# Kernel tuning notes

Measured on AMD Instinct MI355X. Metric: run time of the kernel, lower is better.

Reference implementation:

```python
import jax, jax.numpy as jnp
import numpy as np
import math

B, N, T, CI, CO = 4, 2048, 64, 32, 32
K, TAU = 6, 3


def _cheb(x, gso, k_order):
    # x: [b,n,t,c] complex, gso: [n,n] complex -> [K,b,n,t,c]
    polys = [x]
    if k_order > 1:
        polys.append(jnp.einsum('nm,bmtc->bntc', gso, x))
    for _ in range(2, k_order):
        polys.append(2.0 * jnp.einsum('nm,bmtc->bntc', gso, polys[-1]) - polys[-2])
    return jnp.stack(polys)


def _lag(p, tau):
    # shift along time axis (-2) by tau, zero-padding at the front
    if tau == 0:
        return p
    pad = jnp.zeros_like(p[..., :tau, :])
    return jnp.concatenate([pad, p[..., :-tau, :]], axis=-2)


def setup_inputs() -> dict:
    key = jax.random.key(0)
    ks = jax.random.split(key, 6)
    scale = 1.0 / math.sqrt(K * TAU * CI)
    gso_scale = 0.5 / math.sqrt(N)  # keep spectral radius ~<=1 for Cheb recursion
    return {
        'x_real': jax.random.normal(ks[0], (B, N, T, CI), jnp.float32),
        'x_imag': jax.random.normal(ks[1], (B, N, T, CI), jnp.float32),
        'gso_real': jax.random.normal(ks[2], (N, N), jnp.float32) * gso_scale,
        'gso_imag': jax.random.normal(ks[3], (N, N), jnp.float32) * gso_scale,
        'weight_real': jax.random.uniform(ks[4], (K, TAU, CI, CO), jnp.float32, -scale, scale),
        'weight_imag': jax.random.uniform(ks[5], (K, TAU, CI, CO), jnp.float32, -scale, scale),
        'bias_real': jnp.zeros((CO,), jnp.float32),
        'bias_imag': jnp.zeros((CO,), jnp.float32),
    }


def reference(x_real, x_imag, gso_real, gso_imag, weight_real, weight_imag, bias_real, bias_imag):
    x = jax.lax.complex(x_real, x_imag)
    gso = jax.lax.complex(gso_real, gso_imag)
    w = jax.lax.complex(weight_real, weight_imag)  # [K,TAU,i,o]
    bias = jax.lax.complex(bias_real, bias_imag)
    # Lag (time shift) and the graph shift act on different axes, so they
    # commute: compute the Chebyshev recursion ONCE on x, then lag the
    # stacked polynomials — same math as cheb(lag(x)) in the original.
    polys = _cheb(x, gso, K)  # [K,b,n,t,c]
    out = jnp.zeros((B, N, T, CO), dtype=polys.dtype)
    for tau in range(TAU):
        out = out + jnp.einsum('kbnti,kio->bnto', _lag(polys, tau), w[:, tau])
    return out + bias
```

## Files before the change

kernel.cpp:

```cpp
#include <hip/hip_runtime.h>
#include <stdint.h>

#define Bn 4
#define Nn 2048
#define Tn 64
#define CIn 32
#define COn 32
#define Kn 6
#define TAUn 3
#define Jn 8192

typedef _Float16 f16;
typedef _Float16 f16x2 __attribute__((ext_vector_type(2)));
typedef _Float16 f16x4 __attribute__((ext_vector_type(4)));
typedef _Float16 f16x8 __attribute__((ext_vector_type(8)));
typedef float f32x4 __attribute__((ext_vector_type(4)));

template <int N> struct ic { static constexpr int v = N; };

#if defined(__has_builtin)
#if __has_builtin(__builtin_amdgcn_fdot2)
#define HAVE_FDOT2 1
#endif
#endif

__device__ __forceinline__ float fdot2(f16x2 a, f16x2 b, float c) {
#ifdef HAVE_FDOT2
  return __builtin_amdgcn_fdot2(a, b, c, false);
#else
  return c + (float)a[0] * (float)b[0] + (float)a[1] * (float)b[1];
#endif
}

__device__ __forceinline__ void gld_lds16(const void* g, void* l) {
  auto gp = (const __attribute__((address_space(1))) uint32_t*)(uintptr_t)g;
  auto lp = (__attribute__((address_space(3))) uint32_t*)(uint32_t)(uintptr_t)l;
  __builtin_amdgcn_global_load_lds(gp, lp, 16, 0, 0);
}

__global__ __launch_bounds__(256) void pack_gso(const float* __restrict__ gr,
                                                const float* __restrict__ gi,
                                                f16* __restrict__ Gr,
                                                f16* __restrict__ Gi) {
  int u = blockIdx.x * 256 + threadIdx.x;
  float4 vr = ((const float4*)gr)[u];
  float4 vi = ((const float4*)gi)[u];
  f16x4 hr, hi;
  hr[0] = (f16)vr.x; hr[1] = (f16)vr.y; hr[2] = (f16)vr.z; hr[3] = (f16)vr.w;
  hi[0] = (f16)vi.x; hi[1] = (f16)vi.y; hi[2] = (f16)vi.z; hi[3] = (f16)vi.w;
  ((f16x4*)Gr)[u] = hr;
  ((f16x4*)Gi)[u] = hi;
}

__global__ __launch_bounds__(256) void pack_x(const float* __restrict__ xr,
                                              const float* __restrict__ xi,
                                              f16* __restrict__ P0) {
  __shared__ float tile[64][65];
  const int t = threadIdx.x;
  const int q0 = blockIdx.x * 64;
  const int n0 = blockIdx.y * 64;
  const int b = blockIdx.z;
  const int rr = t >> 4;
  const int cc = (t & 15) * 4;
  #pragma unroll
  for (int plane = 0; plane < 2; ++plane) {
    const float* src = plane ? xi : xr;
    if (plane) __syncthreads();
    #pragma unroll
    for (int it = 0; it < 4; ++it) {
      int n = it * 16 + rr;
      float4 v = *(const float4*)(src + ((size_t)b * Nn + n0 + n) * 2048 + q0 + cc);
      tile[n][cc + 0] = v.x; tile[n][cc + 1] = v.y;
      tile[n][cc + 2] = v.z; tile[n][cc + 3] = v.w;
    }
    __syncthreads();
    #pragma unroll
    for (int it = 0; it < 4; ++it) {
      int q = it * 16 + rr;
      f16x4 hv;
      hv[0] = (f16)tile[cc + 0][q];
      hv[1] = (f16)tile[cc + 1][q];
      hv[2] = (f16)tile[cc + 2][q];
      hv[3] = (f16)tile[cc + 3][q];
      *(f16x4*)(P0 + ((size_t)b * 2048 + q0 + q) * 4096 + plane * 2048 + n0 + cc) = hv;
    }
  }
}

__global__ __launch_bounds__(256) void pack_w(const float* __restrict__ wr,
                                              const float* __restrict__ wi,
                                              uint2* __restrict__ wpk) {
  int idx = blockIdx.x * 256 + threadIdx.x;
  if (idx >= Kn * TAUn * CIn * COn) return;
  float r = wr[idx], i = wi[idx];
  uint16_t hr = __builtin_bit_cast(uint16_t, (f16)r);
  uint16_t hi = __builtin_bit_cast(uint16_t, (f16)i);
  uint16_t hni = __builtin_bit_cast(uint16_t, (f16)(-i));
  uint2 o;
  o.x = (uint32_t)hr | ((uint32_t)hni << 16);
  o.y = (uint32_t)hi | ((uint32_t)hr << 16);
  wpk[idx] = o;
}

template <int MODE>
__global__ __launch_bounds__(256, 2) void cheb_gemm(
    const f16* __restrict__ Gr, const f16* __restrict__ Gi,
    const f16* __restrict__ P, f16* __restrict__ Q) {
  extern __shared__ __align__(16) char lds[];
  f16* L = (f16*)lds;

  const int tid = threadIdx.x;
  const int lane = tid & 63;
  const int w = tid >> 6;
  const int wm = w >> 1;
  const int wn = w & 1;
  const int sub = lane >> 4, rr = lane & 15;

  const int bid = blockIdx.x;
  const int xcd = bid & 7;
  const int l = bid >> 3;
  const int s = l & 63, wv = l >> 6;
  const int bj = xcd * 8 + (s >> 3);
  const int bn = (s & 7) + 8 * wv;
  const int n0 = bn * 128, j0 = bj * 128;
  const bool top = n0 < 2048;
  const int gmbase = n0 & 2047;

  const int trow = tid >> 3;
  const int cg = (tid & 7) ^ (trow & 7);
  const size_t aoffg = (size_t)(gmbase + trow) * 2048 + cg * 8;
  const size_t boffg = (size_t)(j0 + trow) * 4096 + cg * 8;
  const int sdst = w * 512;

  const int arb = rr * 64 + (sub ^ (rr & 3)) * 8;
  const int x32 = ((rr >> 2) & 1) * 32;
  const int kofs[2] = {x32, 32 - x32};

  auto stageA = [&](const f16* plane, int kcol, int h, int slot) {
    #pragma unroll
    for (int p = 0; p < 2; ++p)
      gld_lds16(plane + aoffg + h * 131072 + p * 65536 + kcol,
                L + slot * 4096 + sdst + p * 2048);
  };
  auto stageB = [&](int kt_, int h, int slot) {
    #pragma unroll
    for (int p = 0; p < 2; ++p)
      gld_lds16(P + boffg + h * 262144 + p * 131072 + kt_ * 64,
                L + slot * 4096 + sdst + p * 2048);
  };
  auto Aplane = [&](int kt_) -> const f16* {
    bool kr = (kt_ & 32) != 0;
    return top ? (kr ? Gi : Gr) : (kr ? Gr : Gi);
  };

  f32x4 acc[4][4] = {};
  f16x8 afr[2][2], bfr0[2][2], bfr1[2][2];

  stageB(0, 0, 2);
  stageA(Aplane(0), 0, 0, 0);
  stageA(Aplane(0), 0, 1, 1);
  stageB(0, 1, 3);
  stageB(1, 0, 6);
  stageA(Aplane(1), 64, 0, 4);

  for (int k2 = 0; k2 < 32; ++k2) {
    const int ktb = k2 * 2;

    auto tile = [&](auto ec) {
      constexpr int E = decltype(ec)::v;
      const int kt = ktb + E;
      const int ktn = (kt + 1) & 63;
      const int ktn2 = (kt + 2) & 63;
      const f16* apn = Aplane(ktn);
      const f16* apn2 = Aplane(ktn2);
      const int kcoln = (ktn * 64) & 2047;
      const int kcoln2 = (ktn2 * 64) & 2047;
      const bool negA = top && (kt & 32);

      auto loadA = [&](int qm) {
        #pragma unroll
        for (int f = 0; f < 2; ++f)
          #pragma unroll
          for (int ks = 0; ks < 2; ++ks)
            afr[f][ks] = *(const f16x8*)(
                L + (E * 4 + wm) * 4096 + qm * 2048 + f * 1024 + arb + kofs[ks]);
        if (negA) {
          #pragma unroll
          for (int f = 0; f < 2; ++f) { afr[f][0] = -afr[f][0]; afr[f][1] = -afr[f][1]; }
        }
      };
      auto loadB = [&](f16x8 (&bq)[2][2], int qn) {
        #pragma unroll
        for (int fc = 0; fc < 2; ++fc)
          #pragma unroll
          for (int ks = 0; ks < 2; ++ks)
            bq[fc][ks] = *(const f16x8*)(
                L + (E * 4 + 2 + wn) * 4096 + qn * 2048 + fc * 1024 + arb + kofs[ks]);
      };
      auto mf16 = [&](f16x8 (&bq)[2][2], int accR, int accC) {
        __builtin_amdgcn_s_setprio(1);
        #pragma unroll
        for (int ks = 0; ks < 2; ++ks)
          #pragma unroll
          for (int f = 0; f < 2; ++f)
            #pragma unroll
            for (int fc = 0; fc < 2; ++fc)
              acc[accR + f][accC + fc] = __builtin_amdgcn_mfma_f32_16x16x32_f16(
                  afr[f][ks], bq[fc][ks], acc[accR + f][accC + fc], 0, 0, 0);
        __builtin_amdgcn_s_setprio(0);
      };

      asm volatile("s_waitcnt vmcnt(4)" ::: "memory");
      __builtin_amdgcn_s_barrier();

      loadA(0); loadB(bfr0, 0);
      stageA(apn, kcoln, 1, (E ^ 1) * 4 + 1);
      mf16(bfr0, 0, 0);

      loadB(bfr1, 1);
      stageB(ktn, 1, (E ^ 1) * 4 + 3);
      mf16(bfr1, 0, 2);

      loadA(1);
      asm volatile("s_waitcnt lgkmcnt(0)" ::: "memory");
      __builtin_amdgcn_s_barrier();
      stageB(ktn2, 0, E * 4 + 2);
      mf16(bfr1, 2, 2);

      stageA(apn2, kcoln2, 0, E * 4 + 0);
      mf16(bfr0, 2, 0);
    };

    tile(ic<0>{});
    tile(ic<1>{});
  }

  asm volatile("s_waitcnt vmcnt(0)" ::: "memory");

  #pragma unroll
  for (int fc = 0; fc < 4; ++fc) {
    size_t j = (size_t)j0 + wn * 64 + fc * 16 + (lane & 15);
    #pragma unroll
    for (int fr = 0; fr < 4; ++fr) {
      int nn = n0 + wm * 64 + fr * 16 + ((lane >> 4) << 2);
      size_t off = j * 4096 + nn;
      f16x4 v;
      if (MODE == 1) {
        f16x4 o = *(const f16x4*)(Q + off);
        #pragma unroll
        for (int r = 0; r < 4; ++r)
          v[r] = (f16)(2.0f * acc[fr][fc][r] - (float)o[r]);
      } else {
        #pragma unroll
        for (int r = 0; r < 4; ++r)
          v[r] = (f16)acc[fr][fc][r];
      }
      *(f16x4*)(Q + off) = v;
    }
  }
}

template <bool CPLX>
__global__ __launch_bounds__(256, 2) void contract_k(
    const f16* __restrict__ Pc, const uint2* __restrict__ wpk,
    const float* __restrict__ biasr, const float* __restrict__ biasi,
    float* __restrict__ out, int k) {
  __shared__ __align__(16) uint32_t Plds[192 * 64];
  __shared__ __align__(16) uint32_t WA[96 * 32];
  __shared__ __align__(16) uint32_t WB[CPLX ? 96 * 32 : 32];

  const int t = threadIdx.x;
  const int n0 = blockIdx.x * 64;
  const int t0 = blockIdx.y * 4;
  const int b = blockIdx.z;

  #pragma unroll
  for (int it = 0; it < 6; ++it) {
    int task = it * 256 + t;
    int row = task >> 3, oc = task & 7;
    int tp = (t0 - 2) * 32 + row;
    uint4 ur = {0, 0, 0, 0}, ui = {0, 0, 0, 0};
    if (tp >= 0) {
      size_t goff = ((size_t)b * 2048 + tp) * 4096 + n0 + oc * 8;
      ur = *(const uint4*)(Pc + goff);
      ui = *(const uint4*)(Pc + goff + 2048);
    }
    uint32_t* dst = &Plds[row * 64 + oc * 8];
    dst[0] = (ur.x & 0xffffu) | (ui.x << 16);
    dst[1] = (ur.x >> 16) | (ui.x & 0xffff0000u);
    dst[2] = (ur.y & 0xffffu) | (ui.y << 16);
    dst[3] = (ur.y >> 16) | (ui.y & 0xffff0000u);
    dst[4] = (ur.z & 0xffffu) | (ui.z << 16);
    dst[5] = (ur.z >> 16) | (ui.z & 0xffff0000u);
    dst[6] = (ur.w & 0xffffu) | (ui.w << 16);
    dst[7] = (ur.w >> 16) | (ui.w & 0xffff0000u);
  }
  #pragma unroll
  for (int it = 0; it < 12; ++it) {
    int idx = it * 256 + t;
    int q = idx >> 5, o = idx & 31;
    int tau = 2 - (q >> 5), ci = q & 31;
    uint2 wv = wpk[((k * TAUn + tau) * CIn + ci) * COn + o];
    WA[idx] = wv.x;
    if (CPLX) WB[idx] = wv.y;
  }
  __syncthreads();

  const int no = t & 7, ng = t >> 3;
  float aR[4][8] = {};
  float aI[4][8] = {};
  for (int q = 0; q < 96; ++q) {
    uint4 wa = *(const uint4*)&WA[q * 32 + no * 4];
    const uint32_t* wap = &wa.x;
    uint4 wb;
    const uint32_t* wbp = &wb.x;
    if (CPLX) wb = *(const uint4*)&WB[q * 32 + no * 4];
    #pragma unroll
    for (int ts = 0; ts < 4; ++ts) {
      uint2 pp = *(const uint2*)&Plds[(ts * 32 + q) * 64 + ng * 2];
      f16x2 h0 = __builtin_bit_cast(f16x2, pp.x);
      f16x2 h1 = __builtin_bit_cast(f16x2, pp.y);
      #pragma unroll
      for (int c = 0; c < 4; ++c) {
        f16x2 wv = __builtin_bit_cast(f16x2, wap[c]);
        aR[ts][c] = fdot2(h0, wv, aR[ts][c]);
        aR[ts][4 + c] = fdot2(h1, wv, aR[ts][4 + c]);
      }
      if (CPLX) {
        #pragma unroll
        for (int c = 0; c < 4; ++c) {
          f16x2 wv = __builtin_bit_cast(f16x2, wbp[c]);
          aI[ts][c] = fdot2(h0, wv, aI[ts][c]);
          aI[ts][4 + c] = fdot2(h1, wv, aI[ts][4 + c]);
        }
      }
    }
  }

  #pragma unroll
  for (int ts = 0; ts < 4; ++ts) {
    const int tt = t0 + ts;
    #pragma unroll
    for (int a = 0; a < 2; ++a) {
      size_t n = (size_t)n0 + ng * 2 + a;
      size_t ob = (((size_t)b * Nn + n) * Tn + tt) * COn + no * 4;
      if (!CPLX) {
        float4 v;
        v.x = aR[ts][a * 4 + 0]; v.y = aR[ts][a * 4 + 1];
        v.z = aR[ts][a * 4 + 2]; v.w = aR[ts][a * 4 + 3];
        float4 cur;
        if (k == 0) cur = *(const float4*)(biasr + no * 4);
        else cur = *(const float4*)(out + ob);
        v.x += cur.x; v.y += cur.y; v.z += cur.z; v.w += cur.w;
        *(float4*)(out + ob) = v;
      } else {
        float* po = out + ob * 2;
        float4 lo, hi;
        lo.x = aR[ts][a * 4 + 0]; lo.y = aI[ts][a * 4 + 0];
        lo.z = aR[ts][a * 4 + 1]; lo.w = aI[ts][a * 4 + 1];
        hi.x = aR[ts][a * 4 + 2]; hi.y = aI[ts][a * 4 + 2];
        hi.z = aR[ts][a * 4 + 3]; hi.w = aI[ts][a * 4 + 3];
        float4 c0, c1;
        if (k == 0) {
          const float* pr = biasr + no * 4;
          const float* pi = biasi + no * 4;
          c0 = make_float4(pr[0], pi[0], pr[1], pi[1]);
          c1 = make_float4(pr[2], pi[2], pr[3], pi[3]);
        } else {
          c0 = *(const float4*)(po);
          c1 = *(const float4*)(po + 4);
        }
        lo.x += c0.x; lo.y += c0.y; lo.z += c0.z; lo.w += c0.w;
        hi.x += c1.x; hi.y += c1.y; hi.z += c1.z; hi.w += c1.w;
        *(float4*)(po) = lo;
        *(float4*)(po + 4) = hi;
      }
    }
  }
}

extern "C" void kernel_launch(void* const* d_in, const int* in_sizes, int n_in,
                              void* d_out, int out_size, void* d_ws, size_t ws_size,
                              hipStream_t stream) {
  (void)in_sizes; (void)n_in;
  const float* xr = (const float*)d_in[0];
  const float* xi = (const float*)d_in[1];
  const float* gr = (const float*)d_in[2];
  const float* gi = (const float*)d_in[3];
  const float* wr = (const float*)d_in[4];
  const float* wi = (const float*)d_in[5];
  const float* biasr = (const float*)d_in[6];
  const float* biasi = (const float*)d_in[7];
  float* out = (float*)d_out;

  const size_t PPLANE = (size_t)Jn * 4096 * sizeof(f16);
  const size_t GPLANE = (size_t)Nn * Nn * sizeof(f16);
  const size_t WPK = (size_t)Kn * TAUn * CIn * COn * 8;
  if (ws_size < 2 * PPLANE + 2 * GPLANE + WPK) return;

  char* ws = (char*)d_ws;
  f16* P0 = (f16*)(ws);
  f16* P1 = (f16*)(ws + PPLANE);
  f16* Gr = (f16*)(ws + 2 * PPLANE);
  f16* Gi = (f16*)(ws + 2 * PPLANE + GPLANE);
  uint2* wpk = (uint2*)(ws + 2 * PPLANE + 2 * GPLANE);

  const bool cplx = (out_size == 2 * Bn * Nn * Tn * COn);

  pack_gso<<<dim3(4096), dim3(256), 0, stream>>>(gr, gi, Gr, Gi);
  pack_x<<<dim3(32, 32, 4), dim3(256), 0, stream>>>(xr, xi, P0);
  pack_w<<<dim3(72), dim3(256), 0, stream>>>(wr, wi, wpk);

  #define CONTRACT(KK, Pp)                                                         \
    do {                                                                           \
      if (cplx)                                                                    \
        contract_k<true><<<dim3(32, 16, 4), dim3(256), 0, stream>>>(               \
            Pp, wpk, biasr, biasi, out, KK);                                       \
      else                                                                         \
        contract_k<false><<<dim3(32, 16, 4), dim3(256), 0, stream>>>(              \
            Pp, wpk, biasr, biasi, out, KK);                                       \
    } while (0)

  CONTRACT(0, P0);
  cheb_gemm<0><<<dim3(2048), dim3(256), 65536, stream>>>(Gr, Gi, P0, P1);
  CONTRACT(1, P1);
  cheb_gemm<1><<<dim3(2048), dim3(256), 65536, stream>>>(Gr, Gi, P1, P0);
  CONTRACT(2, P0);
  cheb_gemm<1><<<dim3(2048), dim3(256), 65536, stream>>>(Gr, Gi, P0, P1);
  CONTRACT(3, P1);
  cheb_gemm<1><<<dim3(2048), dim3(256), 65536, stream>>>(Gr, Gi, P1, P0);
  CONTRACT(4, P0);
  cheb_gemm<1><<<dim3(2048), dim3(256), 65536, stream>>>(Gr, Gi, P0, P1);
  CONTRACT(5, P1);
  #undef CONTRACT
}
```

Baseline: 1.891 ms.

## Halve cheb_gemm K-tile and LDS footprint to raise occupancy to four blocks

The Chebyshev GEMM now stages 32-wide K tiles in a two-slot double buffer instead of 64-wide tiles in a more elaborately interleaved four-way staging scheme, halving dynamic LDS to 32KB. Launch bounds move from two to four blocks per CU so that more waves can hide memory latency. Each tile loads all A/B fragments, then issues a 4x4 block of MFMAs in one burst. The trade-off is twice as many loop iterations and barriers per output tile, and the loss of fine-grained overlap between LDS reads, global staging and MFMA issue. The tighter register cap may also cause spills.

Result: slower. 2.175 ms (+15.0%).

```diff
diff --git a/kernel.cpp b/kernel.cpp
--- a/kernel.cpp
+++ b/kernel.cpp
@@ -103,7 +103,7 @@
 }
 
 template <int MODE>
-__global__ __launch_bounds__(256, 2) void cheb_gemm(
+__global__ __launch_bounds__(256, 4) void cheb_gemm(
     const f16* __restrict__ Gr, const f16* __restrict__ Gi,
     const f16* __restrict__ P, f16* __restrict__ Q) {
   extern __shared__ __align__(16) char lds[];
@@ -126,109 +126,77 @@
   const bool top = n0 < 2048;
   const int gmbase = n0 & 2047;
 
-  const int trow = tid >> 3;
-  const int cg = (tid & 7) ^ (trow & 7);
-  const size_t aoffg = (size_t)(gmbase + trow) * 2048 + cg * 8;
-  const size_t boffg = (size_t)(j0 + trow) * 4096 + cg * 8;
+  const int srow = tid >> 2;
+  const int kcg = (tid & 3) ^ ((tid >> 3) & 3);
+  const size_t aoffg = (size_t)(gmbase + srow) * 2048 + kcg * 8;
+  const size_t boffg = (size_t)(j0 + srow) * 4096 + kcg * 8;
   const int sdst = w * 512;
 
-  const int arb = rr * 64 + (sub ^ (rr & 3)) * 8;
-  const int x32 = ((rr >> 2) & 1) * 32;
-  const int kofs[2] = {x32, 32 - x32};
-
-  auto stageA = [&](const f16* plane, int kcol, int h, int slot) {
+  const int arb = rr * 32 + (sub ^ ((rr >> 1) & 3)) * 8;
+
+  auto stageA = [&](const f16* plane, int kcol, int slot) {
     #pragma unroll
     for (int p = 0; p < 2; ++p)
-      gld_lds16(plane + aoffg + h * 131072 + p * 65536 + kcol,
-                L + slot * 4096 + sdst + p * 2048);
+      gld_lds16(plane + aoffg + p * 131072 + kcol,
+                L + slot * 4096 + p * 2048 + sdst);
   };
-  auto stageB = [&](int kt_, int h, int slot) {
+  auto stageB = [&](int kt_, int slot) {
     #pragma unroll
     for (int p = 0; p < 2; ++p)
-      gld_lds16(P + boffg + h * 262144 + p * 131072 + kt_ * 64,
-                L + slot * 4096 + sdst + p * 2048);
+      gld_lds16(P + boffg + p * 262144 + kt_ * 32,
+                L + slot * 4096 + p * 2048 + sdst);
   };
   auto Aplane = [&](int kt_) -> const f16* {
-    bool kr = (kt_ & 32) != 0;
+    bool kr = (kt_ & 64) != 0;
     return top ? (kr ? Gi : Gr) : (kr ? Gr : Gi);
   };
 
   f32x4 acc[4][4] = {};
-  f16x8 afr[2][2], bfr0[2][2], bfr1[2][2];
-
-  stageB(0, 0, 2);
-  stageA(Aplane(0), 0, 0, 0);
-  stageA(Aplane(0), 0, 1, 1);
-  stageB(0, 1, 3);
-  stageB(1, 0, 6);
-  stageA(Aplane(1), 64, 0, 4);
-
-  for (int k2 = 0; k2 < 32; ++k2) {
+  f16x8 afr[4], bfr[4];
+
+  stageA(Aplane(0), 0, 0);
+  stageB(0, 2);
+  stageA(Aplane(1), 32, 1);
+  stageB(1, 3);
+
+  for (int k2 = 0; k2 < 64; ++k2) {
     const int ktb = k2 * 2;
 
     auto tile = [&](auto ec) {
       constexpr int E = decltype(ec)::v;
       const int kt = ktb + E;
-      const int ktn = (kt + 1) & 63;
-      const int ktn2 = (kt + 2) & 63;
-      const f16* apn = Aplane(ktn);
+      const int ktn2 = (kt + 2) & 127;
       const f16* apn2 = Aplane(ktn2);
-      const int kcoln = (ktn * 64) & 2047;
-      const int kcoln2 = (ktn2 * 64) & 2047;
-      const bool negA = top && (kt & 32);
-
-      auto loadA = [&](int qm) {
-        #pragma unroll
-        for (int f = 0; f < 2; ++f)
-          #pragma unroll
-          for (int ks = 0; ks < 2; ++ks)
-            afr[f][ks] = *(const f16x8*)(
-                L + (E * 4 + wm) * 4096 + qm * 2048 + f * 1024 + arb + kofs[ks]);
-        if (negA) {
-          #pragma unroll
-          for (int f = 0; f < 2; ++f) { afr[f][0] = -afr[f][0]; afr[f][1] = -afr[f][1]; }
-        }
-      };
-      auto loadB = [&](f16x8 (&bq)[2][2], int qn) {
-        #pragma unroll
-        for (int fc = 0; fc < 2; ++fc)
-          #pragma unroll
-          for (int ks = 0; ks < 2; ++ks)
-            bq[fc][ks] = *(const f16x8*)(
-                L + (E * 4 + 2 + wn) * 4096 + qn * 2048 + fc * 1024 + arb + kofs[ks]);
-      };
-      auto mf16 = [&](f16x8 (&bq)[2][2], int accR, int accC) {
-        __builtin_amdgcn_s_setprio(1);
-        #pragma unroll
-        for (int ks = 0; ks < 2; ++ks)
-          #pragma unroll
-          for (int f = 0; f < 2; ++f)
-            #pragma unroll
-            for (int fc = 0; fc < 2; ++fc)
-              acc[accR + f][accC + fc] = __builtin_amdgcn_mfma_f32_16x16x32_f16(
-                  afr[f][ks], bq[fc][ks], acc[accR + f][accC + fc], 0, 0, 0);
-        __builtin_amdgcn_s_setprio(0);
-      };
+      const int kcol2 = (ktn2 * 32) & 2047;
+      const bool negA = top && (kt & 64);
 
       asm volatile("s_waitcnt vmcnt(4)" ::: "memory");
       __builtin_amdgcn_s_barrier();
 
-      loadA(0); loadB(bfr0, 0);
-      stageA(apn, kcoln, 1, (E ^ 1) * 4 + 1);
-      mf16(bfr0, 0, 0);
-
-      loadB(bfr1, 1);
-      stageB(ktn, 1, (E ^ 1) * 4 + 3);
-      mf16(bfr1, 0, 2);
-
-      loadA(1);
+      #pragma unroll
+      for (int f = 0; f < 4; ++f)
+        afr[f] = *(const f16x8*)(L + E * 4096 + wm * 2048 + f * 512 + arb);
+      #pragma unroll
+      for (int fc = 0; fc < 4; ++fc)
+        bfr[fc] = *(const f16x8*)(L + (2 + E) * 4096 + wn * 2048 + fc * 512 + arb);
+      if (negA) {
+        #pragma unroll
+        for (int f = 0; f < 4; ++f) afr[f] = -afr[f];
+      }
+
       asm volatile("s_waitcnt lgkmcnt(0)" ::: "memory");
       __builtin_amdgcn_s_barrier();
-      stageB(ktn2, 0, E * 4 + 2);
-      mf16(bfr1, 2, 2);
-
-      stageA(apn2, kcoln2, 0, E * 4 + 0);
-      mf16(bfr0, 2, 0);
+      stageA(apn2, kcol2, E);
+      stageB(ktn2, 2 + E);
+
+      __builtin_amdgcn_s_setprio(1);
+      #pragma unroll
+      for (int f = 0; f < 4; ++f)
+        #pragma unroll
+        for (int fc = 0; fc < 4; ++fc)
+          acc[f][fc] = __builtin_amdgcn_mfma_f32_16x16x32_f16(
+              afr[f], bfr[fc], acc[f][fc], 0, 0, 0);
+      __builtin_amdgcn_s_setprio(0);
     };
 
     tile(ic<0>{});
@@ -322,16 +290,16 @@
       f16x2 h1 = __builtin_bit_cast(f16x2, pp.y);
       #pragma unroll
       for (int c = 0; c < 4; ++c) {
-        f16x2 wv = __builtin_bit_cast(f16x2, wap[c]);
-        aR[ts][c] = fdot2(h0, wv, aR[ts][c]);
-        aR[ts][4 + c] = fdot2(h1, wv, aR[ts][4 + c]);
+        f16x2 wvv = __builtin_bit_cast(f16x2, wap[c]);
+        aR[ts][c] = fdot2(h0, wvv, aR[ts][c]);
+        aR[ts][4 + c] = fdot2(h1, wvv, aR[ts][4 + c]);
       }
       if (CPLX) {
         #pragma unroll
         for (int c = 0; c < 4; ++c) {
-          f16x2 wv = __builtin_bit_cast(f16x2, wbp[c]);
-          aI[ts][c] = fdot2(h0, wv, aI[ts][c]);
-          aI[ts][4 + c] = fdot2(h1, wv, aI[ts][4 + c]);
+          f16x2 wvv = __builtin_bit_cast(f16x2, wbp[c]);
+          aI[ts][c] = fdot2(h0, wvv, aI[ts][c]);
+          aI[ts][4 + c] = fdot2(h1, wvv, aI[ts][4 + c]);
         }
       }
     }
@@ -422,15 +390,15 @@
     } while (0)
 
   CONTRACT(0, P0);
-  cheb_gemm<0><<<dim3(2048), dim3(256), 65536, stream>>>(Gr, Gi, P0, P1);
+  cheb_gemm<0><<<dim3(2048), dim3(256), 32768, stream>>>(Gr, Gi, P0, P1);
   CONTRACT(1, P1);
-  cheb_gemm<1><<<dim3(2048), dim3(256), 65536, stream>>>(Gr, Gi, P1, P0);
+  cheb_gemm<1><<<dim3(2048), dim3(256), 32768, stream>>>(Gr, Gi, P1, P0);
   CONTRACT(2, P0);
-  cheb_gemm<1><<<dim3(2048), dim3(256), 65536, stream>>>(Gr, Gi, P0, P1);
+  cheb_gemm<1><<<dim3(2048), dim3(256), 32768, stream>>>(Gr, Gi, P0, P1);
   CONTRACT(3, P1);
-  cheb_gemm<1><<<dim3(2048), dim3(256), 65536, stream>>>(Gr, Gi, P1, P0);
+  cheb_gemm<1><<<dim3(2048), dim3(256), 32768, stream>>>(Gr, Gi, P1, P0);
   CONTRACT(4, P0);
-  cheb_gemm<1><<<dim3(2048), dim3(256), 65536, stream>>>(Gr, Gi, P0, P1);
+  cheb_gemm<1><<<dim3(2048), dim3(256), 32768, stream>>>(Gr, Gi, P0, P1);
   CONTRACT(5, P1);
   #undef CONTRACT
 }
```

## Pre-pack GSO into MFMA fragment layout and load A directly to registers

Applied to the files above, without the earlier changes.

The graph-shift matrix is repacked into 16x32 MFMA fragment order so each wave can load its A operands straight from global memory into registers, bypassing LDS. LDS is then used only for the B operand, which halves dynamic shared memory and removes A-side LDS reads and stores. The per-tile schedule is simplified into one block of MFMAs with A prefetched two tiles ahead. The cost is more VGPRs for the double-buffered A fragments and a global-load latency that must be hidden by the deeper prefetch.

Result: slower. 1.995 ms (+5.5%).

```diff
diff --git a/kernel.cpp b/kernel.cpp
--- a/kernel.cpp
+++ b/kernel.cpp
@@ -38,18 +38,27 @@
   __builtin_amdgcn_global_load_lds(gp, lp, 16, 0, 0);
 }
 
+__device__ __forceinline__ void gload16(f16x8& d, const f16* p) {
+  asm volatile("global_load_dwordx4 %0, %1, off" : "=v"(d) : "v"(p) : "memory");
+}
+
 __global__ __launch_bounds__(256) void pack_gso(const float* __restrict__ gr,
                                                 const float* __restrict__ gi,
-                                                f16* __restrict__ Gr,
-                                                f16* __restrict__ Gi) {
-  int u = blockIdx.x * 256 + threadIdx.x;
-  float4 vr = ((const float4*)gr)[u];
-  float4 vi = ((const float4*)gi)[u];
-  f16x4 hr, hi;
-  hr[0] = (f16)vr.x; hr[1] = (f16)vr.y; hr[2] = (f16)vr.z; hr[3] = (f16)vr.w;
-  hi[0] = (f16)vi.x; hi[1] = (f16)vi.y; hi[2] = (f16)vi.z; hi[3] = (f16)vi.w;
-  ((f16x4*)Gr)[u] = hr;
-  ((f16x4*)Gi)[u] = hi;
+                                                f16* __restrict__ Gpr,
+                                                f16* __restrict__ Gpi) {
+  int idx = blockIdx.x * 256 + threadIdx.x;
+  int l = idx & 63;
+  int e = idx >> 6;
+  int n16 = e >> 6, k32 = e & 63;
+  int row = n16 * 16 + (l & 15);
+  int col = k32 * 32 + (l >> 4) * 8;
+  const float* sr = gr + (size_t)row * 2048 + col;
+  const float* si = gi + (size_t)row * 2048 + col;
+  f16x8 hr, hi;
+  #pragma unroll
+  for (int j = 0; j < 8; ++j) { hr[j] = (f16)sr[j]; hi[j] = (f16)si[j]; }
+  *(f16x8*)(Gpr + (size_t)e * 512 + l * 8) = hr;
+  *(f16x8*)(Gpi + (size_t)e * 512 + l * 8) = hi;
 }
 
 __global__ __launch_bounds__(256) void pack_x(const float* __restrict__ xr,
@@ -104,7 +113,7 @@
 
 template <int MODE>
 __global__ __launch_bounds__(256, 2) void cheb_gemm(
-    const f16* __restrict__ Gr, const f16* __restrict__ Gi,
+    const f16* __restrict__ Gpr, const f16* __restrict__ Gpi,
     const f16* __restrict__ P, f16* __restrict__ Q) {
   extern __shared__ __align__(16) char lds[];
   f16* L = (f16*)lds;
@@ -125,10 +134,10 @@
   const int n0 = bn * 128, j0 = bj * 128;
   const bool top = n0 < 2048;
   const int gmbase = n0 & 2047;
+  const int n16base = (gmbase >> 4) + wm * 4;
 
   const int trow = tid >> 3;
   const int cg = (tid & 7) ^ (trow & 7);
-  const size_t aoffg = (size_t)(gmbase + trow) * 2048 + cg * 8;
   const size_t boffg = (size_t)(j0 + trow) * 4096 + cg * 8;
   const int sdst = w * 512;
 
@@ -136,32 +145,36 @@
   const int x32 = ((rr >> 2) & 1) * 32;
   const int kofs[2] = {x32, 32 - x32};
 
-  auto stageA = [&](const f16* plane, int kcol, int h, int slot) {
-    #pragma unroll
-    for (int p = 0; p < 2; ++p)
-      gld_lds16(plane + aoffg + h * 131072 + p * 65536 + kcol,
-                L + slot * 4096 + sdst + p * 2048);
-  };
   auto stageB = [&](int kt_, int h, int slot) {
     #pragma unroll
     for (int p = 0; p < 2; ++p)
       gld_lds16(P + boffg + h * 262144 + p * 131072 + kt_ * 64,
-                L + slot * 4096 + sdst + p * 2048);
+                L + slot * 4096 + p * 2048 + sdst);
   };
   auto Aplane = [&](int kt_) -> const f16* {
     bool kr = (kt_ & 32) != 0;
-    return top ? (kr ? Gi : Gr) : (kr ? Gr : Gi);
+    return top ? (kr ? Gpi : Gpr) : (kr ? Gpr : Gpi);
   };
 
   f32x4 acc[4][4] = {};
-  f16x8 afr[2][2], bfr0[2][2], bfr1[2][2];
-
-  stageB(0, 0, 2);
-  stageA(Aplane(0), 0, 0, 0);
-  stageA(Aplane(0), 0, 1, 1);
-  stageB(0, 1, 3);
-  stageB(1, 0, 6);
-  stageA(Aplane(1), 64, 0, 4);
+  f16x8 afr[2][4][2];
+  f16x8 bfr0[2][2], bfr1[2][2];
+
+  auto loadAfr = [&](int E_, int kt_) {
+    const f16* pl = Aplane(kt_);
+    const int k2b = (kt_ & 31) * 2;
+    #pragma unroll
+    for (int f4 = 0; f4 < 4; ++f4)
+      #pragma unroll
+      for (int ks = 0; ks < 2; ++ks)
+        gload16(afr[E_][f4][ks],
+                pl + ((size_t)(n16base + f4) * 64 + k2b + ks) * 512 + lane * 8);
+  };
+
+  stageB(0, 0, 0); stageB(0, 1, 1);
+  loadAfr(0, 0);
+  stageB(1, 0, 2); stageB(1, 1, 3);
+  loadAfr(1, 1);
 
   for (int k2 = 0; k2 < 32; ++k2) {
     const int ktb = k2 * 2;
@@ -169,66 +182,56 @@
     auto tile = [&](auto ec) {
       constexpr int E = decltype(ec)::v;
       const int kt = ktb + E;
-      const int ktn = (kt + 1) & 63;
       const int ktn2 = (kt + 2) & 63;
-      const f16* apn = Aplane(ktn);
-      const f16* apn2 = Aplane(ktn2);
-      const int kcoln = (ktn * 64) & 2047;
-      const int kcoln2 = (ktn2 * 64) & 2047;
       const bool negA = top && (kt & 32);
 
-      auto loadA = [&](int qm) {
-        #pragma unroll
-        for (int f = 0; f < 2; ++f)
-          #pragma unroll
-          for (int ks = 0; ks < 2; ++ks)
-            afr[f][ks] = *(const f16x8*)(
-                L + (E * 4 + wm) * 4096 + qm * 2048 + f * 1024 + arb + kofs[ks]);
-        if (negA) {
-          #pragma unroll
-          for (int f = 0; f < 2; ++f) { afr[f][0] = -afr[f][0]; afr[f][1] = -afr[f][1]; }
-        }
-      };
       auto loadB = [&](f16x8 (&bq)[2][2], int qn) {
         #pragma unroll
         for (int fc = 0; fc < 2; ++fc)
           #pragma unroll
           for (int ks = 0; ks < 2; ++ks)
             bq[fc][ks] = *(const f16x8*)(
-                L + (E * 4 + 2 + wn) * 4096 + qn * 2048 + fc * 1024 + arb + kofs[ks]);
+                L + (E * 2 + wn) * 4096 + qn * 2048 + fc * 1024 + arb + kofs[ks]);
       };
-      auto mf16 = [&](f16x8 (&bq)[2][2], int accR, int accC) {
-        __builtin_amdgcn_s_setprio(1);
+
+      asm volatile("s_waitcnt vmcnt(12)" ::: "memory");
+      __builtin_amdgcn_s_barrier();
+      __builtin_amdgcn_sched_barrier(0);
+
+      loadB(bfr0, 0);
+      loadB(bfr1, 1);
+      if (negA) {
+        #pragma unroll
+        for (int f4 = 0; f4 < 4; ++f4) {
+          afr[E][f4][0] = -afr[E][f4][0];
+          afr[E][f4][1] = -afr[E][f4][1];
+        }
+      }
+
+      asm volatile("s_waitcnt lgkmcnt(0)" ::: "memory");
+      __builtin_amdgcn_s_barrier();
+      stageB(ktn2, 0, E * 2);
+      stageB(ktn2, 1, E * 2 + 1);
+
+      __builtin_amdgcn_s_setprio(1);
+      #pragma unroll
+      for (int qm = 0; qm < 2; ++qm)
         #pragma unroll
         for (int ks = 0; ks < 2; ++ks)
           #pragma unroll
-          for (int f = 0; f < 2; ++f)
+          for (int f = 0; f < 2; ++f) {
             #pragma unroll
             for (int fc = 0; fc < 2; ++fc)
-              acc[accR + f][accC + fc] = __builtin_amdgcn_mfma_f32_16x16x32_f16(
-                  afr[f][ks], bq[fc][ks], acc[accR + f][accC + fc], 0, 0, 0);
-        __builtin_amdgcn_s_setprio(0);
-      };
-
-      asm volatile("s_waitcnt vmcnt(4)" ::: "memory");
-      __builtin_amdgcn_s_barrier();
-
-      loadA(0); loadB(bfr0, 0);
-      stageA(apn, kcoln, 1, (E ^ 1) * 4 + 1);
-      mf16(bfr0, 0, 0);
-
-      loadB(bfr1, 1);
-      stageB(ktn, 1, (E ^ 1) * 4 + 3);
-      mf16(bfr1, 0, 2);
-
-      loadA(1);
-      asm volatile("s_waitcnt lgkmcnt(0)" ::: "memory");
-      __builtin_amdgcn_s_barrier();
-      stageB(ktn2, 0, E * 4 + 2);
-      mf16(bfr1, 2, 2);
-
-      stageA(apn2, kcoln2, 0, E * 4 + 0);
-      mf16(bfr0, 2, 0);
+              acc[qm * 2 + f][fc] = __builtin_amdgcn_mfma_f32_16x16x32_f16(
+                  afr[E][qm * 2 + f][ks], bfr0[fc][ks], acc[qm * 2 + f][fc], 0, 0, 0);
+            #pragma unroll
+            for (int fc = 0; fc < 2; ++fc)
+              acc[qm * 2 + f][2 + fc] = __builtin_amdgcn_mfma_f32_16x16x32_f16(
+                  afr[E][qm * 2 + f][ks], bfr1[fc][ks], acc[qm * 2 + f][2 + fc], 0, 0, 0);
+          }
+      __builtin_amdgcn_s_setprio(0);
+
+      loadAfr(E, ktn2);
     };
 
     tile(ic<0>{});
@@ -322,16 +325,16 @@
       f16x2 h1 = __builtin_bit_cast(f16x2, pp.y);
       #pragma unroll
       for (int c = 0; c < 4; ++c) {
-        f16x2 wv = __builtin_bit_cast(f16x2, wap[c]);
-        aR[ts][c] = fdot2(h0, wv, aR[ts][c]);
-        aR[ts][4 + c] = fdot2(h1, wv, aR[ts][4 + c]);
+        f16x2 wvv = __builtin_bit_cast(f16x2, wap[c]);
+        aR[ts][c] = fdot2(h0, wvv, aR[ts][c]);
+        aR[ts][4 + c] = fdot2(h1, wvv, aR[ts][4 + c]);
       }
       if (CPLX) {
         #pragma unroll
         for (int c = 0; c < 4; ++c) {
-          f16x2 wv = __builtin_bit_cast(f16x2, wbp[c]);
-          aI[ts][c] = fdot2(h0, wv, aI[ts][c]);
-          aI[ts][4 + c] = fdot2(h1, wv, aI[ts][4 + c]);
+          f16x2 wvv = __builtin_bit_cast(f16x2, wbp[c]);
+          aI[ts][c] = fdot2(h0, wvv, aI[ts][c]);
+          aI[ts][4 + c] = fdot2(h1, wvv, aI[ts][4 + c]);
         }
       }
     }
@@ -401,13 +404,13 @@
   char* ws = (char*)d_ws;
   f16* P0 = (f16*)(ws);
   f16* P1 = (f16*)(ws + PPLANE);
-  f16* Gr = (f16*)(ws + 2 * PPLANE);
-  f16* Gi = (f16*)(ws + 2 * PPLANE + GPLANE);
+  f16* Gpr = (f16*)(ws + 2 * PPLANE);
+  f16* Gpi = (f16*)(ws + 2 * PPLANE + GPLANE);
   uint2* wpk = (uint2*)(ws + 2 * PPLANE + 2 * GPLANE);
 
   const bool cplx = (out_size == 2 * Bn * Nn * Tn * COn);
 
-  pack_gso<<<dim3(4096), dim3(256), 0, stream>>>(gr, gi, Gr, Gi);
+  pack_gso<<<dim3(2048), dim3(256), 0, stream>>>(gr, gi, Gpr, Gpi);
   pack_x<<<dim3(32, 32, 4), dim3(256), 0, stream>>>(xr, xi, P0);
   pack_w<<<dim3(72), dim3(256), 0, stream>>>(wr, wi, wpk);
 
@@ -422,15 +425,15 @@
     } while (0)
 
   CONTRACT(0, P0);
-  cheb_gemm<0><<<dim3(2048), dim3(256), 65536, stream>>>(Gr, Gi, P0, P1);
+  cheb_gemm<0><<<dim3(2048), dim3(256), 32768, stream>>>(Gpr, Gpi, P0, P1);
   CONTRACT(1, P1);
-  cheb_gemm<1><<<dim3(2048), dim3(256), 65536, stream>>>(Gr, Gi, P1, P0);
+  cheb_gemm<1><<<dim3(2048), dim3(256), 32768, stream>>>(Gpr, Gpi, P1, P0);
   CONTRACT(2, P0);
-  cheb_gemm<1><<<dim3(2048), dim3(256), 65536, stream>>>(Gr, Gi, P0, P1);
+  cheb_gemm<1><<<dim3(2048), dim3(256), 32768, stream>>>(Gpr, Gpi, P0, P1);
   CONTRACT(3, P1);
-  cheb_gemm<1><<<dim3(2048), dim3(256), 65536, stream>>>(Gr, Gi, P1, P0);
+  cheb_gemm<1><<<dim3(2048), dim3(256), 32768, stream>>>(Gpr, Gpi, P1, P0);
   CONTRACT(4, P0);
-  cheb_gemm<1><<<dim3(2048), dim3(256), 65536, stream>>>(Gr, Gi, P0, P1);
+  cheb_gemm<1><<<dim3(2048), dim3(256), 32768, stream>>>(Gpr, Gpi, P0, P1);
   CONTRACT(5, P1);
   #undef CONTRACT
 }
```
